# Performance work log

Hardware: AMD Instinct MI355X
Metric: run time of the kernel (lower is better)

The kernel has to match this reference:

```python
import jax, jax.numpy as jnp
import numpy as np

N = 50000
E = 800000
D_IN = 128
H = 128
D_OUT = 64
BN_EPS = 1e-5


def setup_inputs() -> dict:
    key = jax.random.key(0)
    ks = jax.random.split(key, 20)

    def lin(k, fin, fout):
        kw, kb = jax.random.split(k)
        w = jax.random.normal(kw, (fin, fout), jnp.float32) / np.sqrt(fin)
        b = jnp.zeros((fout,), jnp.float32)
        return w, b

    def bn_params(k, d):
        kg, kb = jax.random.split(k)
        g = 1.0 + 0.1 * jax.random.normal(kg, (d,), jnp.float32)
        b = 0.1 * jax.random.normal(kb, (d,), jnp.float32)
        rm = 0.1 * jax.random.normal(jax.random.fold_in(k, 7), (d,), jnp.float32)
        rv = jnp.abs(1.0 + 0.1 * jax.random.normal(jax.random.fold_in(k, 9), (d,), jnp.float32))
        return g, b, rm, rv

    x = jax.random.normal(ks[0], (N, D_IN), jnp.float32)
    edge_index = jax.random.randint(ks[1], (2, E), 0, N, jnp.int64)
    ricci_curvature = jax.random.normal(ks[2], (E,), jnp.float32)

    W1, b1 = lin(ks[3], D_IN, H)
    Wc0, bc0 = lin(ks[4], H, H)          # convs[0]: hidden*1 -> hidden
    Wc1, bc1 = lin(ks[5], 2 * H, H)      # convs[1]: hidden*2 -> hidden
    Wout, bout = lin(ks[6], 3 * H, D_OUT)  # conv2: hidden*(L-1) -> out

    bn1_g, bn1_b, bn1_rm, bn1_rv = bn_params(ks[7], D_IN)
    bnc0_g, bnc0_b, bnc0_rm, bnc0_rv = bn_params(ks[8], H)
    bnc1_g, bnc1_b, bnc1_rm, bnc1_rv = bn_params(ks[9], 2 * H)
    bn2_g, bn2_b, bn2_rm, bn2_rv = bn_params(ks[10], 3 * H)

    return {
        "x": x, "edge_index": edge_index, "percent": 50,
        "ricci_curvature": ricci_curvature,
        "W1": W1, "b1": b1, "Wc0": Wc0, "bc0": bc0,
        "Wc1": Wc1, "bc1": bc1, "Wout": Wout, "bout": bout,
        "bn1_g": bn1_g, "bn1_b": bn1_b, "bn1_rm": bn1_rm, "bn1_rv": bn1_rv,
        "bnc0_g": bnc0_g, "bnc0_b": bnc0_b, "bnc0_rm": bnc0_rm, "bnc0_rv": bnc0_rv,
        "bnc1_g": bnc1_g, "bnc1_b": bnc1_b, "bnc1_rm": bnc1_rm, "bnc1_rv": bnc1_rv,
        "bn2_g": bn2_g, "bn2_b": bn2_b, "bn2_rm": bn2_rm, "bn2_rv": bn2_rv,
    }


def _bn_eval(h, g, b, rm, rv):
    # BatchNorm1d in eval mode: affine normalize with running stats.
    return (h - rm) * (g * jax.lax.rsqrt(rv + BN_EPS)) + b


def reference(x, edge_index, percent, ricci_curvature,
              W1, b1, Wc0, bc0, Wc1, bc1, Wout, bout,
              bn1_g, bn1_b, bn1_rm, bn1_rv,
              bnc0_g, bnc0_b, bnc0_rm, bnc0_rv,
              bnc1_g, bnc1_b, bnc1_rm, bnc1_rv,
              bn2_g, bn2_b, bn2_rm, bn2_rv):
    n = x.shape[0]
    # GCN normalization with self-loops (PyG GCNConv default), shared by all layers
    loops = jnp.arange(n, dtype=edge_index.dtype)
    row = jnp.concatenate([edge_index[0], loops])  # source
    col = jnp.concatenate([edge_index[1], loops])  # target
    deg = jax.ops.segment_sum(jnp.ones_like(col, dtype=x.dtype), col, num_segments=n)
    dinv = jax.lax.rsqrt(deg)  # deg >= 1 thanks to self loops
    norm = (dinv[row] * dinv[col])[:, None]  # [E+N, 1]

    def gcn(h, W, b):
        hw = h @ W                                   # transform first (PyG order)
        msg = hw[row] * norm                          # gather + scale per edge
        return jax.ops.segment_sum(msg, col, num_segments=n) + b

    # eval mode: no sampling / dynamic reweighting, dropout = identity
    h = _bn_eval(x, bn1_g, bn1_b, bn1_rm, bn1_rv)
    h = jax.nn.relu(gcn(h, W1, b1))
    r0 = h

    h = _bn_eval(h, bnc0_g, bnc0_b, bnc0_rm, bnc0_rv)
    h = jax.nn.relu(gcn(h, Wc0, bc0))
    r1 = h
    h = jnp.concatenate([r0, r1], axis=1)  # [N, 2H]

    h = _bn_eval(h, bnc1_g, bnc1_b, bnc1_rm, bnc1_rv)
    h = jax.nn.relu(gcn(h, Wc1, bc1))
    r2 = h
    h = jnp.concatenate([r0, r1, r2], axis=1)  # [N, 3H]

    h = _bn_eval(h, bn2_g, bn2_b, bn2_rm, bn2_rv)
    out = gcn(h, Wout, bout)
    return (out, r0, r1, r2)
```

## Files before the change

### kernel.cpp

```cpp
#include <hip/hip_runtime.h>
#include <hip/hip_bf16.h>
#include <stdint.h>

#define NN 50000
#define NE 800000

typedef unsigned short ushort8 __attribute__((ext_vector_type(8)));
typedef __bf16 bf16x8 __attribute__((ext_vector_type(8)));
typedef float f32x4 __attribute__((ext_vector_type(4)));

__device__ __forceinline__ float bf2f_bits(unsigned short u) {
  unsigned int x = ((unsigned int)u) << 16;
  float f;
  __builtin_memcpy(&f, &x, 4);
  return f;
}
__device__ __forceinline__ unsigned short f2bf_bits(float f) {
  unsigned int x;
  __builtin_memcpy(&x, &f, 4);
  unsigned int lsb = (x >> 16) & 1u;
  x += 0x7fffu + lsb;
  return (unsigned short)(x >> 16);
}
__device__ __forceinline__ float loadf(const void* base, size_t idx, int isbf) {
  if (isbf) return bf2f_bits(((const unsigned short*)base)[idx]);
  return ((const float*)base)[idx];
}

__global__ void k_sniff(const void* x, const void* ei, int* flags) {
  __shared__ int badbf;
  __shared__ int zodd;
  int tid = threadIdx.x;
  if (tid == 0) { badbf = 0; zodd = 0; }
  __syncthreads();
  unsigned short u = ((const unsigned short*)x)[tid];
  float v = bf2f_bits(u);
  float av = fabsf(v);
  int ok = (av == 0.0f) || (av > 1e-8f && av < 1e8f);
  if (!ok) atomicAdd(&badbf, 1);
  int e32 = ((const int*)ei)[tid];
  if ((tid & 1) && e32 == 0) atomicAdd(&zodd, 1);
  __syncthreads();
  if (tid == 0) {
    flags[0] = (badbf <= 12) ? 1 : 0;
    flags[1] = (zodd >= 100) ? 1 : 0;
  }
}

__global__ void k_cvt_edges(const void* ei, int* erow, int* ecol, int* rank,
                            int* cnt, const int* flags) {
  int e = blockIdx.x * 256 + threadIdx.x;
  if (e >= NE) return;
  int r, c;
  if (flags[1]) {
    const long long* p = (const long long*)ei;
    r = (int)p[e];
    c = (int)p[NE + e];
  } else {
    const int* p = (const int*)ei;
    r = p[e];
    c = p[NE + e];
  }
  erow[e] = r;
  ecol[e] = c;
  rank[e] = atomicAdd(&cnt[c], 1);
}

__global__ void k_cvt_xb(const void* x, unsigned short* xb, const int* flags) {
  int i4 = (blockIdx.x * 256 + threadIdx.x) * 4;
  if (i4 >= NN * 128) return;
  int isbf = flags[0];
  if (isbf) {
    *reinterpret_cast<uint2*>(xb + i4) =
        *reinterpret_cast<const uint2*>((const unsigned short*)x + i4);
  } else {
    float4 v = *reinterpret_cast<const float4*>((const float*)x + i4);
    xb[i4 + 0] = f2bf_bits(v.x); xb[i4 + 1] = f2bf_bits(v.y);
    xb[i4 + 2] = f2bf_bits(v.z); xb[i4 + 3] = f2bf_bits(v.w);
  }
}

__global__ void k_zero_int(int* p, int n) {
  int i = blockIdx.x * 256 + threadIdx.x;
  if (i < n) p[i] = 0;
}
__global__ void k_scan1(const int* cnt, int* indptr, int* bsum, float* dinv, int n) {
  __shared__ int sm[256];
  int tid = threadIdx.x;
  int i = blockIdx.x * 256 + tid;
  int v = (i < n) ? cnt[i] : 0;
  if (i < n) dinv[i] = rsqrtf((float)(v + 1));
  sm[tid] = v;
  __syncthreads();
  for (int off = 1; off < 256; off <<= 1) {
    int t = (tid >= off) ? sm[tid - off] : 0;
    __syncthreads();
    sm[tid] += t;
    __syncthreads();
  }
  if (i < n) indptr[i] = sm[tid] - v;
  if (tid == 255) bsum[blockIdx.x] = sm[255];
}
__global__ void k_scan2(int* bsum, int nb) {
  __shared__ int sm[256];
  int tid = threadIdx.x;
  int v = (tid < nb) ? bsum[tid] : 0;
  sm[tid] = v;
  __syncthreads();
  for (int off = 1; off < 256; off <<= 1) {
    int t = (tid >= off) ? sm[tid - off] : 0;
    __syncthreads();
    sm[tid] += t;
    __syncthreads();
  }
  if (tid < nb) bsum[tid] = sm[tid] - v;
  if (tid == 0) bsum[nb] = sm[255];
}
__global__ void k_scan3(int* indptr, const int* bsum, int n, int nb) {
  int i = blockIdx.x * 256 + threadIdx.x;
  if (i < n) indptr[i] += bsum[i >> 8];
  else if (i == n) indptr[n] = bsum[nb];
}
__global__ void k_fill(const int* erow, const int* ecol, const int* rank,
                       const int* indptr, int* srcs) {
  int e = blockIdx.x * 256 + threadIdx.x;
  if (e >= NE) return;
  srcs[indptr[ecol[e]] + rank[e]] = erow[e];
}

__global__ void k_prep_wt_all(
    const void* W1, const void* Wc0, const void* Wc1, const void* Wout,
    const void* g1, const void* g2, const void* g3, const void* g4,
    const void* rv1, const void* rv2, const void* rv3, const void* rv4,
    unsigned short* Wtb, const int* flags) {
  int idx = blockIdx.x * 256 + threadIdx.x;
  if (idx >= 90112) return;
  int isbf = flags[0];
  const void *W, *g, *rv;
  int K, NOUT, base;
  if (idx < 16384)      { W = W1;   g = g1; rv = rv1; K = 128; NOUT = 128; base = 0; }
  else if (idx < 32768) { W = Wc0;  g = g2; rv = rv2; K = 128; NOUT = 128; base = 16384; }
  else if (idx < 65536) { W = Wc1;  g = g3; rv = rv3; K = 256; NOUT = 128; base = 32768; }
  else                  { W = Wout; g = g4; rv = rv4; K = 384; NOUT = 64;  base = 65536; }
  int li = idx - base;
  int j = li / K, k = li % K;
  float s = loadf(g, k, isbf) * rsqrtf(loadf(rv, k, isbf) + 1e-5f);
  Wtb[idx] = f2bf_bits(s * loadf(W, (size_t)k * NOUT + j, isbf));
}
__global__ void k_prep_c_all(
    const void* W1, const void* Wc0, const void* Wc1, const void* Wout,
    const void* g1, const void* g2, const void* g3, const void* g4,
    const void* b1, const void* b2, const void* b3, const void* b4,
    const void* rm1, const void* rm2, const void* rm3, const void* rm4,
    const void* rv1, const void* rv2, const void* rv3, const void* rv4,
    float* cvec, const int* flags) {
  int jj = blockIdx.x;
  int lane = threadIdx.x;
  int isbf = flags[0];
  const void *W, *g, *bb, *rm, *rv;
  int K, NOUT, j;
  if (jj < 128)      { W = W1;   g = g1; bb = b1; rm = rm1; rv = rv1; K = 128; NOUT = 128; j = jj; }
  else if (jj < 256) { W = Wc0;  g = g2; bb = b2; rm = rm2; rv = rv2; K = 128; NOUT = 128; j = jj - 128; }
  else if (jj < 384) { W = Wc1;  g = g3; bb = b3; rm = rm3; rv = rv3; K = 256; NOUT = 128; j = jj - 256; }
  else               { W = Wout; g = g4; bb = b4; rm = rm4; rv = rv4; K = 384; NOUT = 64;  j = jj - 384; }
  float acc = 0.f;
  for (int k = lane; k < K; k += 64) {
    float s = loadf(g, k, isbf) * rsqrtf(loadf(rv, k, isbf) + 1e-5f);
    float t = loadf(bb, k, isbf) - loadf(rm, k, isbf) * s;
    acc += t * loadf(W, (size_t)k * NOUT + j, isbf);
  }
#pragma unroll
  for (int off = 32; off; off >>= 1) acc += __shfl_down(acc, off);
  if (lane == 0) cvec[jj] = acc;
}

template <int NOUT, int K>
__global__ __launch_bounds__(256) void k_gemm_mfma(
    const unsigned short* __restrict__ h0, const unsigned short* __restrict__ h1,
    const unsigned short* __restrict__ h2, const unsigned short* __restrict__ Wtb,
    const float* __restrict__ cvec, const float* __restrict__ dinv,
    unsigned short* __restrict__ hb) {
  constexpr int KS = K / 32;
  constexpr int NT = NOUT / 16;
  int tid = threadIdx.x;
  int wv = tid >> 6, lane = tid & 63;
  int row0 = blockIdx.x * 64 + wv * 16;
  int l15 = lane & 15;
  int kq = lane >> 4;
  int arow = row0 + l15;
  bool inb = arow < NN;

  bf16x8 afrag[KS];
#pragma unroll
  for (int ks = 0; ks < KS; ++ks) {
    int kg = ks * 32 + kq * 8;
    const unsigned short* src = (kg >> 7) == 0 ? h0 : ((kg >> 7) == 1 ? h1 : h2);
    ushort8 u = (ushort8)0;
    if (inb) u = *reinterpret_cast<const ushort8*>(src + (size_t)arow * 128 + (kg & 127));
    afrag[ks] = __builtin_bit_cast(bf16x8, u);
  }

  f32x4 acc[NT];
#pragma unroll
  for (int nt = 0; nt < NT; ++nt) acc[nt] = (f32x4)0.f;

#pragma unroll
  for (int nt = 0; nt < NT; ++nt) {
    const unsigned short* wrow = Wtb + (size_t)(nt * 16 + l15) * K + kq * 8;
#pragma unroll
    for (int ks = 0; ks < KS; ++ks) {
      ushort8 u = *reinterpret_cast<const ushort8*>(wrow + ks * 32);
      acc[nt] = __builtin_amdgcn_mfma_f32_16x16x32_bf16(
          afrag[ks], __builtin_bit_cast(bf16x8, u), acc[nt], 0, 0, 0);
    }
  }

  int orow0 = row0 + kq * 4;
  float dv[4];
  bool ob[4];
#pragma unroll
  for (int r = 0; r < 4; ++r) {
    int orow = orow0 + r;
    ob[r] = orow < NN;
    dv[r] = ob[r] ? dinv[orow] : 0.f;
  }
#pragma unroll
  for (int nt = 0; nt < NT; ++nt) {
    int col = nt * 16 + l15;
    float cv = cvec[col];
#pragma unroll
    for (int r = 0; r < 4; ++r) {
      if (ob[r])
        hb[(size_t)(orow0 + r) * NOUT + col] = f2bf_bits(dv[r] * (acc[nt][r] + cv));
    }
  }
}

template <int DPL, bool RELU>
__global__ __launch_bounds__(256) void k_agg(
    const unsigned short* __restrict__ hb, const int* __restrict__ indptr,
    const int* __restrict__ srcs, const float* __restrict__ dinv,
    const void* __restrict__ bias, void* __restrict__ dout, size_t region_off,
    unsigned short* __restrict__ rb, const int* __restrict__ flags) {
  int gw = blockIdx.x * 8 + (threadIdx.x >> 5);
  int lane = threadIdx.x & 31;
  if (gw >= NN) return;
  int isbf = flags[0];
  int e0 = indptr[gw], e1 = indptr[gw + 1];
  int e = e0;
  float dv = dinv[gw];

  if constexpr (DPL == 2) {
    size_t co = (size_t)lane * 4;
    uint2 sv = *reinterpret_cast<const uint2*>(hb + (size_t)gw * 128 + co);
    float a0 = bf2f_bits((unsigned short)sv.x), a1 = bf2f_bits((unsigned short)(sv.x >> 16));
    float a2 = bf2f_bits((unsigned short)sv.y), a3 = bf2f_bits((unsigned short)(sv.y >> 16));
    float b0 = 0.f, b1 = 0.f, b2 = 0.f, b3 = 0.f;
    float c0 = 0.f, c1 = 0.f, c2 = 0.f, c3 = 0.f;
    float d0 = 0.f, d1 = 0.f, d2 = 0.f, d3 = 0.f;
    for (; e + 3 < e1; e += 4) {
      int sa = srcs[e], sb = srcs[e + 1], sc = srcs[e + 2], sd = srcs[e + 3];
      uint2 va = *reinterpret_cast<const uint2*>(hb + (size_t)sa * 128 + co);
      uint2 vb = *reinterpret_cast<const uint2*>(hb + (size_t)sb * 128 + co);
      uint2 vc = *reinterpret_cast<const uint2*>(hb + (size_t)sc * 128 + co);
      uint2 vd = *reinterpret_cast<const uint2*>(hb + (size_t)sd * 128 + co);
      a0 += bf2f_bits((unsigned short)va.x); a1 += bf2f_bits((unsigned short)(va.x >> 16));
      a2 += bf2f_bits((unsigned short)va.y); a3 += bf2f_bits((unsigned short)(va.y >> 16));
      b0 += bf2f_bits((unsigned short)vb.x); b1 += bf2f_bits((unsigned short)(vb.x >> 16));
      b2 += bf2f_bits((unsigned short)vb.y); b3 += bf2f_bits((unsigned short)(vb.y >> 16));
      c0 += bf2f_bits((unsigned short)vc.x); c1 += bf2f_bits((unsigned short)(vc.x >> 16));
      c2 += bf2f_bits((unsigned short)vc.y); c3 += bf2f_bits((unsigned short)(vc.y >> 16));
      d0 += bf2f_bits((unsigned short)vd.x); d1 += bf2f_bits((unsigned short)(vd.x >> 16));
      d2 += bf2f_bits((unsigned short)vd.y); d3 += bf2f_bits((unsigned short)(vd.y >> 16));
    }
    for (; e < e1; ++e) {
      int sa = srcs[e];
      uint2 va = *reinterpret_cast<const uint2*>(hb + (size_t)sa * 128 + co);
      a0 += bf2f_bits((unsigned short)va.x); a1 += bf2f_bits((unsigned short)(va.x >> 16));
      a2 += bf2f_bits((unsigned short)va.y); a3 += bf2f_bits((unsigned short)(va.y >> 16));
    }
    float o0 = dv * ((a0 + b0) + (c0 + d0)) + loadf(bias, co + 0, isbf);
    float o1 = dv * ((a1 + b1) + (c1 + d1)) + loadf(bias, co + 1, isbf);
    float o2 = dv * ((a2 + b2) + (c2 + d2)) + loadf(bias, co + 2, isbf);
    float o3 = dv * ((a3 + b3) + (c3 + d3)) + loadf(bias, co + 3, isbf);
    if (RELU) {
      o0 = fmaxf(o0, 0.f); o1 = fmaxf(o1, 0.f);
      o2 = fmaxf(o2, 0.f); o3 = fmaxf(o3, 0.f);
    }
    size_t eo = region_off + (size_t)gw * 128 + co;
    uint2 pk;
    pk.x = (unsigned int)f2bf_bits(o0) | ((unsigned int)f2bf_bits(o1) << 16);
    pk.y = (unsigned int)f2bf_bits(o2) | ((unsigned int)f2bf_bits(o3) << 16);
    if (isbf) {
      *reinterpret_cast<uint2*>((unsigned short*)dout + eo) = pk;
    } else {
      float4 fo; fo.x = o0; fo.y = o1; fo.z = o2; fo.w = o3;
      *reinterpret_cast<float4*>((float*)dout + eo) = fo;
    }
    if (rb) *reinterpret_cast<uint2*>(rb + (size_t)gw * 128 + co) = pk;
  } else {
    size_t co = (size_t)lane * 2;
    unsigned int sv = *reinterpret_cast<const unsigned int*>(hb + (size_t)gw * 64 + co);
    float a0 = bf2f_bits((unsigned short)sv), a1 = bf2f_bits((unsigned short)(sv >> 16));
    float b0 = 0.f, b1 = 0.f, c0 = 0.f, c1 = 0.f, d0 = 0.f, d1 = 0.f;
    for (; e + 3 < e1; e += 4) {
      int sa = srcs[e], sb = srcs[e + 1], sc = srcs[e + 2], sd = srcs[e + 3];
      unsigned int va = *reinterpret_cast<const unsigned int*>(hb + (size_t)sa * 64 + co);
      unsigned int vb = *reinterpret_cast<const unsigned int*>(hb + (size_t)sb * 64 + co);
      unsigned int vc = *reinterpret_cast<const unsigned int*>(hb + (size_t)sc * 64 + co);
      unsigned int vd = *reinterpret_cast<const unsigned int*>(hb + (size_t)sd * 64 + co);
      a0 += bf2f_bits((unsigned short)va); a1 += bf2f_bits((unsigned short)(va >> 16));
      b0 += bf2f_bits((unsigned short)vb); b1 += bf2f_bits((unsigned short)(vb >> 16));
      c0 += bf2f_bits((unsigned short)vc); c1 += bf2f_bits((unsigned short)(vc >> 16));
      d0 += bf2f_bits((unsigned short)vd); d1 += bf2f_bits((unsigned short)(vd >> 16));
    }
    for (; e < e1; ++e) {
      int sa = srcs[e];
      unsigned int va = *reinterpret_cast<const unsigned int*>(hb + (size_t)sa * 64 + co);
      a0 += bf2f_bits((unsigned short)va); a1 += bf2f_bits((unsigned short)(va >> 16));
    }
    float o0 = dv * ((a0 + b0) + (c0 + d0)) + loadf(bias, co + 0, isbf);
    float o1 = dv * ((a1 + b1) + (c1 + d1)) + loadf(bias, co + 1, isbf);
    if (RELU) { o0 = fmaxf(o0, 0.f); o1 = fmaxf(o1, 0.f); }
    size_t eo = region_off + (size_t)gw * 64 + co;
    if (isbf) {
      unsigned int pk = (unsigned int)f2bf_bits(o0) | ((unsigned int)f2bf_bits(o1) << 16);
      *reinterpret_cast<unsigned int*>((unsigned short*)dout + eo) = pk;
    } else {
      float2 fo; fo.x = o0; fo.y = o1;
      *reinterpret_cast<float2*>((float*)dout + eo) = fo;
    }
    if (rb) {
      unsigned int pk = (unsigned int)f2bf_bits(o0) | ((unsigned int)f2bf_bits(o1) << 16);
      *reinterpret_cast<unsigned int*>(rb + (size_t)gw * 64 + co) = pk;
    }
  }
}

extern "C" void kernel_launch(void* const* d_in, const int* in_sizes, int n_in,
                              void* d_out, int out_size, void* d_ws, size_t ws_size,
                              hipStream_t stream) {
  const void* x    = d_in[0];
  const void* ei   = d_in[1];
  const void* W1   = d_in[4];
  const void* b1   = d_in[5];
  const void* Wc0  = d_in[6];
  const void* bc0  = d_in[7];
  const void* Wc1  = d_in[8];
  const void* bc1  = d_in[9];
  const void* Wout = d_in[10];
  const void* bout = d_in[11];
  const void *bn1g = d_in[12], *bn1b = d_in[13], *bn1rm = d_in[14], *bn1rv = d_in[15];
  const void *bc0g = d_in[16], *bc0b = d_in[17], *bc0rm = d_in[18], *bc0rv = d_in[19];
  const void *bc1g = d_in[20], *bc1b = d_in[21], *bc1rm = d_in[22], *bc1rv = d_in[23];
  const void *bn2g = d_in[24], *bn2b = d_in[25], *bn2rm = d_in[26], *bn2rv = d_in[27];
  (void)in_sizes; (void)n_in; (void)out_size; (void)ws_size;

  char* w = (char*)d_ws;
  auto carve = [&](size_t bytes) {
    char* p = w;
    w += (bytes + 255) & ~(size_t)255;
    return p;
  };
  int*   flags  = (int*)  carve(256);
  float* dinv   = (float*)carve(sizeof(float) * NN);
  int*   cnt    = (int*)  carve(sizeof(int) * NN);
  int*   indptr = (int*)  carve(sizeof(int) * (NN + 1));
  int*   bsum   = (int*)  carve(sizeof(int) * 256);
  int*   erow   = (int*)  carve(sizeof(int) * NE);
  int*   ecol   = (int*)  carve(sizeof(int) * NE);
  int*   rank   = (int*)  carve(sizeof(int) * NE);
  int*   srcs   = (int*)  carve(sizeof(int) * NE);
  unsigned short* Wtb = (unsigned short*)carve(sizeof(short) * 90112);
  float* cvec   = (float*)carve(sizeof(float) * 448);
  unsigned short* xb  = (unsigned short*)carve(sizeof(short) * (size_t)NN * 128);
  unsigned short* hb  = (unsigned short*)carve(sizeof(short) * (size_t)NN * 128);
  unsigned short* rb0 = (unsigned short*)carve(sizeof(short) * (size_t)NN * 128);
  unsigned short* rb1 = (unsigned short*)carve(sizeof(short) * (size_t)NN * 128);
  unsigned short* rb2 = (unsigned short*)carve(sizeof(short) * (size_t)NN * 128);

  const int gN = (NN + 255) / 256;
  const int gE = (NE + 255) / 256;
  const int nb = (NN + 255) / 256;
  const int gG = (NN + 63) / 64;
  const int gA = (NN + 7) / 8;

  k_sniff<<<1, 256, 0, stream>>>(x, ei, flags);
  k_zero_int<<<gN, 256, 0, stream>>>(cnt, NN);
  k_cvt_edges<<<gE, 256, 0, stream>>>(ei, erow, ecol, rank, cnt, flags);
  k_cvt_xb<<<(NN * 128 / 4 + 255) / 256, 256, 0, stream>>>(x, xb, flags);
  k_scan1<<<nb, 256, 0, stream>>>(cnt, indptr, bsum, dinv, NN);
  k_scan2<<<1, 256, 0, stream>>>(bsum, nb);
  k_scan3<<<(NN + 1 + 255) / 256, 256, 0, stream>>>(indptr, bsum, NN, nb);
  k_fill<<<gE, 256, 0, stream>>>(erow, ecol, rank, indptr, srcs);
  k_prep_wt_all<<<(90112 + 255) / 256, 256, 0, stream>>>(
      W1, Wc0, Wc1, Wout, bn1g, bc0g, bc1g, bn2g, bn1rv, bc0rv, bc1rv, bn2rv, Wtb, flags);
  k_prep_c_all<<<448, 64, 0, stream>>>(
      W1, Wc0, Wc1, Wout, bn1g, bc0g, bc1g, bn2g, bn1b, bc0b, bc1b, bn2b,
      bn1rm, bc0rm, bc1rm, bn2rm, bn1rv, bc0rv, bc1rv, bn2rv, cvec, flags);

  const size_t offO  = 0;
  const size_t offR0 = (size_t)NN * 64;
  const size_t offR1 = offR0 + (size_t)NN * 128;
  const size_t offR2 = offR1 + (size_t)NN * 128;

  k_gemm_mfma<128, 128><<<gG, 256, 0, stream>>>(xb, nullptr, nullptr, Wtb + 0, cvec + 0, dinv, hb);
  k_agg<2, true><<<gA, 256, 0, stream>>>(hb, indptr, srcs, dinv, b1, d_out, offR0, rb0, flags);

  k_gemm_mfma<128, 128><<<gG, 256, 0, stream>>>(rb0, nullptr, nullptr, Wtb + 16384, cvec + 128, dinv, hb);
  k_agg<2, true><<<gA, 256, 0, stream>>>(hb, indptr, srcs, dinv, bc0, d_out, offR1, rb1, flags);

  k_gemm_mfma<128, 256><<<gG, 256, 0, stream>>>(rb0, rb1, nullptr, Wtb + 32768, cvec + 256, dinv, hb);
  k_agg<2, true><<<gA, 256, 0, stream>>>(hb, indptr, srcs, dinv, bc1, d_out, offR2, rb2, flags);

  k_gemm_mfma<64, 384><<<gG, 256, 0, stream>>>(rb0, rb1, rb2, Wtb + 65536, cvec + 384, dinv, hb);
  k_agg<1, false><<<gA, 256, 0, stream>>>(hb, indptr, srcs, dinv, bout, d_out, offO, nullptr, flags);
}
```

Before: 340.4 us.

## Use wave64 per node for 128-wide aggregation and skip redundant bf16 residual copies

The 128-wide aggregation now assigns a full 64-lane wave per node, with each lane handling 2 features and 8 edges unrolled per iteration, where before 32 lanes handled 4 features each. When the output is bf16, the aggregation no longer writes a separate bf16 residual buffer; the following GEMMs read the residuals directly from the output tensor. The count-zeroing kernel is folded into the sniff kernel to save a launch. In exchange, each edge now costs smaller 4-byte gathers per lane and there are more waves per node count.

Measured after the change: 334.4 us. Within noise of the previous version (-1.8%).

```diff
diff --git a/kernel.cpp b/kernel.cpp
--- a/kernel.cpp
+++ b/kernel.cpp
@@ -22,12 +22,17 @@
   x += 0x7fffu + lsb;
   return (unsigned short)(x >> 16);
 }
+__device__ __forceinline__ float lo16(unsigned int v) { return bf2f_bits((unsigned short)v); }
+__device__ __forceinline__ float hi16(unsigned int v) { return bf2f_bits((unsigned short)(v >> 16)); }
 __device__ __forceinline__ float loadf(const void* base, size_t idx, int isbf) {
   if (isbf) return bf2f_bits(((const unsigned short*)base)[idx]);
   return ((const float*)base)[idx];
 }
 
-__global__ void k_sniff(const void* x, const void* ei, int* flags) {
+__global__ void k_sniff(const void* x, const void* ei, int* flags, int* cnt) {
+  int i = blockIdx.x * 256 + threadIdx.x;
+  if (i < NN) cnt[i] = 0;
+  if (blockIdx.x != 0) return;
   __shared__ int badbf;
   __shared__ int zodd;
   int tid = threadIdx.x;
@@ -80,10 +85,6 @@
   }
 }
 
-__global__ void k_zero_int(int* p, int n) {
-  int i = blockIdx.x * 256 + threadIdx.x;
-  if (i < n) p[i] = 0;
-}
 __global__ void k_scan1(const int* cnt, int* indptr, int* bsum, float* dinv, int n) {
   __shared__ int sm[256];
   int tid = threadIdx.x;
@@ -176,12 +177,19 @@
 
 template <int NOUT, int K>
 __global__ __launch_bounds__(256) void k_gemm_mfma(
-    const unsigned short* __restrict__ h0, const unsigned short* __restrict__ h1,
-    const unsigned short* __restrict__ h2, const unsigned short* __restrict__ Wtb,
+    const unsigned short* __restrict__ h0b, const unsigned short* __restrict__ h1b,
+    const unsigned short* __restrict__ h2b,
+    const unsigned short* __restrict__ h0d, const unsigned short* __restrict__ h1d,
+    const unsigned short* __restrict__ h2d,
+    const unsigned short* __restrict__ Wtb,
     const float* __restrict__ cvec, const float* __restrict__ dinv,
-    unsigned short* __restrict__ hb) {
+    unsigned short* __restrict__ hb, const int* __restrict__ flags) {
   constexpr int KS = K / 32;
   constexpr int NT = NOUT / 16;
+  int isbf = flags[0];
+  const unsigned short* h0 = (isbf && h0d) ? h0d : h0b;
+  const unsigned short* h1 = (isbf && h1d) ? h1d : h1b;
+  const unsigned short* h2 = (isbf && h2d) ? h2d : h2b;
   int tid = threadIdx.x;
   int wv = tid >> 6, lane = tid & 63;
   int row0 = blockIdx.x * 64 + wv * 16;
@@ -236,104 +244,98 @@
   }
 }
 
-template <int DPL, bool RELU>
-__global__ __launch_bounds__(256) void k_agg(
+template <bool RELU>
+__global__ __launch_bounds__(256) void k_agg128(
     const unsigned short* __restrict__ hb, const int* __restrict__ indptr,
     const int* __restrict__ srcs, const float* __restrict__ dinv,
     const void* __restrict__ bias, void* __restrict__ dout, size_t region_off,
     unsigned short* __restrict__ rb, const int* __restrict__ flags) {
+  int gw = __builtin_amdgcn_readfirstlane(blockIdx.x * 4 + (threadIdx.x >> 6));
+  int lane = threadIdx.x & 63;
+  if (gw >= NN) return;
+  int isbf = flags[0];
+  int e0 = indptr[gw], e1 = indptr[gw + 1];
+  size_t co = (size_t)lane * 2;
+  unsigned int sv = *reinterpret_cast<const unsigned int*>(hb + (size_t)gw * 128 + co);
+  float a0 = lo16(sv), a1 = hi16(sv);
+  float b0 = 0.f, b1 = 0.f, c0 = 0.f, c1 = 0.f, d0 = 0.f, d1 = 0.f;
+  int e = e0;
+  for (; e + 7 < e1; e += 8) {
+    int s0 = srcs[e], s1 = srcs[e + 1], s2 = srcs[e + 2], s3 = srcs[e + 3];
+    int s4 = srcs[e + 4], s5 = srcs[e + 5], s6 = srcs[e + 6], s7 = srcs[e + 7];
+    unsigned int v0 = *reinterpret_cast<const unsigned int*>(hb + (size_t)s0 * 128 + co);
+    unsigned int v1 = *reinterpret_cast<const unsigned int*>(hb + (size_t)s1 * 128 + co);
+    unsigned int v2 = *reinterpret_cast<const unsigned int*>(hb + (size_t)s2 * 128 + co);
+    unsigned int v3 = *reinterpret_cast<const unsigned int*>(hb + (size_t)s3 * 128 + co);
+    unsigned int v4 = *reinterpret_cast<const unsigned int*>(hb + (size_t)s4 * 128 + co);
+    unsigned int v5 = *reinterpret_cast<const unsigned int*>(hb + (size_t)s5 * 128 + co);
+    unsigned int v6 = *reinterpret_cast<const unsigned int*>(hb + (size_t)s6 * 128 + co);
+    unsigned int v7 = *reinterpret_cast<const unsigned int*>(hb + (size_t)s7 * 128 + co);
+    a0 += lo16(v0); a1 += hi16(v0); b0 += lo16(v1); b1 += hi16(v1);
+    c0 += lo16(v2); c1 += hi16(v2); d0 += lo16(v3); d1 += hi16(v3);
+    a0 += lo16(v4); a1 += hi16(v4); b0 += lo16(v5); b1 += hi16(v5);
+    c0 += lo16(v6); c1 += hi16(v6); d0 += lo16(v7); d1 += hi16(v7);
+  }
+  for (; e < e1; ++e) {
+    int s0 = srcs[e];
+    unsigned int v0 = *reinterpret_cast<const unsigned int*>(hb + (size_t)s0 * 128 + co);
+    a0 += lo16(v0); a1 += hi16(v0);
+  }
+  float dv = dinv[gw];
+  float o0 = dv * ((a0 + b0) + (c0 + d0)) + loadf(bias, co + 0, isbf);
+  float o1 = dv * ((a1 + b1) + (c1 + d1)) + loadf(bias, co + 1, isbf);
+  if (RELU) { o0 = fmaxf(o0, 0.f); o1 = fmaxf(o1, 0.f); }
+  size_t eo = region_off + (size_t)gw * 128 + co;
+  if (isbf) {
+    unsigned int pk = (unsigned int)f2bf_bits(o0) | ((unsigned int)f2bf_bits(o1) << 16);
+    *reinterpret_cast<unsigned int*>((unsigned short*)dout + eo) = pk;
+  } else {
+    float2 fo; fo.x = o0; fo.y = o1;
+    *reinterpret_cast<float2*>((float*)dout + eo) = fo;
+    unsigned int pk = (unsigned int)f2bf_bits(o0) | ((unsigned int)f2bf_bits(o1) << 16);
+    *reinterpret_cast<unsigned int*>(rb + (size_t)gw * 128 + co) = pk;
+  }
+}
+
+__global__ __launch_bounds__(256) void k_agg64out(
+    const unsigned short* __restrict__ hb, const int* __restrict__ indptr,
+    const int* __restrict__ srcs, const float* __restrict__ dinv,
+    const void* __restrict__ bias, void* __restrict__ dout,
+    const int* __restrict__ flags) {
   int gw = blockIdx.x * 8 + (threadIdx.x >> 5);
   int lane = threadIdx.x & 31;
   if (gw >= NN) return;
   int isbf = flags[0];
   int e0 = indptr[gw], e1 = indptr[gw + 1];
   int e = e0;
+  size_t co = (size_t)lane * 2;
+  unsigned int sv = *reinterpret_cast<const unsigned int*>(hb + (size_t)gw * 64 + co);
+  float a0 = lo16(sv), a1 = hi16(sv);
+  float b0 = 0.f, b1 = 0.f, c0 = 0.f, c1 = 0.f, d0 = 0.f, d1 = 0.f;
+  for (; e + 3 < e1; e += 4) {
+    int sa = srcs[e], sb = srcs[e + 1], sc = srcs[e + 2], sd = srcs[e + 3];
+    unsigned int va = *reinterpret_cast<const unsigned int*>(hb + (size_t)sa * 64 + co);
+    unsigned int vb = *reinterpret_cast<const unsigned int*>(hb + (size_t)sb * 64 + co);
+    unsigned int vc = *reinterpret_cast<const unsigned int*>(hb + (size_t)sc * 64 + co);
+    unsigned int vd = *reinterpret_cast<const unsigned int*>(hb + (size_t)sd * 64 + co);
+    a0 += lo16(va); a1 += hi16(va); b0 += lo16(vb); b1 += hi16(vb);
+    c0 += lo16(vc); c1 += hi16(vc); d0 += lo16(vd); d1 += hi16(vd);
+  }
+  for (; e < e1; ++e) {
+    int sa = srcs[e];
+    unsigned int va = *reinterpret_cast<const unsigned int*>(hb + (size_t)sa * 64 + co);
+    a0 += lo16(va); a1 += hi16(va);
+  }
   float dv = dinv[gw];
-
-  if constexpr (DPL == 2) {
-    size_t co = (size_t)lane * 4;
-    uint2 sv = *reinterpret_cast<const uint2*>(hb + (size_t)gw * 128 + co);
-    float a0 = bf2f_bits((unsigned short)sv.x), a1 = bf2f_bits((unsigned short)(sv.x >> 16));
-    float a2 = bf2f_bits((unsigned short)sv.y), a3 = bf2f_bits((unsigned short)(sv.y >> 16));
-    float b0 = 0.f, b1 = 0.f, b2 = 0.f, b3 = 0.f;
-    float c0 = 0.f, c1 = 0.f, c2 = 0.f, c3 = 0.f;
-    float d0 = 0.f, d1 = 0.f, d2 = 0.f, d3 = 0.f;
-    for (; e + 3 < e1; e += 4) {
-      int sa = srcs[e], sb = srcs[e + 1], sc = srcs[e + 2], sd = srcs[e + 3];
-      uint2 va = *reinterpret_cast<const uint2*>(hb + (size_t)sa * 128 + co);
-      uint2 vb = *reinterpret_cast<const uint2*>(hb + (size_t)sb * 128 + co);
-      uint2 vc = *reinterpret_cast<const uint2*>(hb + (size_t)sc * 128 + co);
-      uint2 vd = *reinterpret_cast<const uint2*>(hb + (size_t)sd * 128 + co);
-      a0 += bf2f_bits((unsigned short)va.x); a1 += bf2f_bits((unsigned short)(va.x >> 16));
-      a2 += bf2f_bits((unsigned short)va.y); a3 += bf2f_bits((unsigned short)(va.y >> 16));
-      b0 += bf2f_bits((unsigned short)vb.x); b1 += bf2f_bits((unsigned short)(vb.x >> 16));
-      b2 += bf2f_bits((unsigned short)vb.y); b3 += bf2f_bits((unsigned short)(vb.y >> 16));
-      c0 += bf2f_bits((unsigned short)vc.x); c1 += bf2f_bits((unsigned short)(vc.x >> 16));
-      c2 += bf2f_bits((unsigned short)vc.y); c3 += bf2f_bits((unsigned short)(vc.y >> 16));
-      d0 += bf2f_bits((unsigned short)vd.x); d1 += bf2f_bits((unsigned short)(vd.x >> 16));
-      d2 += bf2f_bits((unsigned short)vd.y); d3 += bf2f_bits((unsigned short)(vd.y >> 16));
-    }
-    for (; e < e1; ++e) {
-      int sa = srcs[e];
-      uint2 va = *reinterpret_cast<const uint2*>(hb + (size_t)sa * 128 + co);
-      a0 += bf2f_bits((unsigned short)va.x); a1 += bf2f_bits((unsigned short)(va.x >> 16));
-      a2 += bf2f_bits((unsigned short)va.y); a3 += bf2f_bits((unsigned short)(va.y >> 16));
-    }
-    float o0 = dv * ((a0 + b0) + (c0 + d0)) + loadf(bias, co + 0, isbf);
-    float o1 = dv * ((a1 + b1) + (c1 + d1)) + loadf(bias, co + 1, isbf);
-    float o2 = dv * ((a2 + b2) + (c2 + d2)) + loadf(bias, co + 2, isbf);
-    float o3 = dv * ((a3 + b3) + (c3 + d3)) + loadf(bias, co + 3, isbf);
-    if (RELU) {
-      o0 = fmaxf(o0, 0.f); o1 = fmaxf(o1, 0.f);
-      o2 = fmaxf(o2, 0.f); o3 = fmaxf(o3, 0.f);
-    }
-    size_t eo = region_off + (size_t)gw * 128 + co;
-    uint2 pk;
-    pk.x = (unsigned int)f2bf_bits(o0) | ((unsigned int)f2bf_bits(o1) << 16);
-    pk.y = (unsigned int)f2bf_bits(o2) | ((unsigned int)f2bf_bits(o3) << 16);
-    if (isbf) {
-      *reinterpret_cast<uint2*>((unsigned short*)dout + eo) = pk;
-    } else {
-      float4 fo; fo.x = o0; fo.y = o1; fo.z = o2; fo.w = o3;
-      *reinterpret_cast<float4*>((float*)dout + eo) = fo;
-    }
-    if (rb) *reinterpret_cast<uint2*>(rb + (size_t)gw * 128 + co) = pk;
+  float o0 = dv * ((a0 + b0) + (c0 + d0)) + loadf(bias, co + 0, isbf);
+  float o1 = dv * ((a1 + b1) + (c1 + d1)) + loadf(bias, co + 1, isbf);
+  size_t eo = (size_t)gw * 64 + co;
+  if (isbf) {
+    unsigned int pk = (unsigned int)f2bf_bits(o0) | ((unsigned int)f2bf_bits(o1) << 16);
+    *reinterpret_cast<unsigned int*>((unsigned short*)dout + eo) = pk;
   } else {
-    size_t co = (size_t)lane * 2;
-    unsigned int sv = *reinterpret_cast<const unsigned int*>(hb + (size_t)gw * 64 + co);
-    float a0 = bf2f_bits((unsigned short)sv), a1 = bf2f_bits((unsigned short)(sv >> 16));
-    float b0 = 0.f, b1 = 0.f, c0 = 0.f, c1 = 0.f, d0 = 0.f, d1 = 0.f;
-    for (; e + 3 < e1; e += 4) {
-      int sa = srcs[e], sb = srcs[e + 1], sc = srcs[e + 2], sd = srcs[e + 3];
-      unsigned int va = *reinterpret_cast<const unsigned int*>(hb + (size_t)sa * 64 + co);
-      unsigned int vb = *reinterpret_cast<const unsigned int*>(hb + (size_t)sb * 64 + co);
-      unsigned int vc = *reinterpret_cast<const unsigned int*>(hb + (size_t)sc * 64 + co);
-      unsigned int vd = *reinterpret_cast<const unsigned int*>(hb + (size_t)sd * 64 + co);
-      a0 += bf2f_bits((unsigned short)va); a1 += bf2f_bits((unsigned short)(va >> 16));
-      b0 += bf2f_bits((unsigned short)vb); b1 += bf2f_bits((unsigned short)(vb >> 16));
-      c0 += bf2f_bits((unsigned short)vc); c1 += bf2f_bits((unsigned short)(vc >> 16));
-      d0 += bf2f_bits((unsigned short)vd); d1 += bf2f_bits((unsigned short)(vd >> 16));
-    }
-    for (; e < e1; ++e) {
-      int sa = srcs[e];
-      unsigned int va = *reinterpret_cast<const unsigned int*>(hb + (size_t)sa * 64 + co);
-      a0 += bf2f_bits((unsigned short)va); a1 += bf2f_bits((unsigned short)(va >> 16));
-    }
-    float o0 = dv * ((a0 + b0) + (c0 + d0)) + loadf(bias, co + 0, isbf);
-    float o1 = dv * ((a1 + b1) + (c1 + d1)) + loadf(bias, co + 1, isbf);
-    if (RELU) { o0 = fmaxf(o0, 0.f); o1 = fmaxf(o1, 0.f); }
-    size_t eo = region_off + (size_t)gw * 64 + co;
-    if (isbf) {
-      unsigned int pk = (unsigned int)f2bf_bits(o0) | ((unsigned int)f2bf_bits(o1) << 16);
-      *reinterpret_cast<unsigned int*>((unsigned short*)dout + eo) = pk;
-    } else {
-      float2 fo; fo.x = o0; fo.y = o1;
-      *reinterpret_cast<float2*>((float*)dout + eo) = fo;
-    }
-    if (rb) {
-      unsigned int pk = (unsigned int)f2bf_bits(o0) | ((unsigned int)f2bf_bits(o1) << 16);
-      *reinterpret_cast<unsigned int*>(rb + (size_t)gw * 64 + co) = pk;
-    }
+    float2 fo; fo.x = o0; fo.y = o1;
+    *reinterpret_cast<float2*>((float*)dout + eo) = fo;
   }
 }
 
@@ -383,10 +385,10 @@
   const int gE = (NE + 255) / 256;
   const int nb = (NN + 255) / 256;
   const int gG = (NN + 63) / 64;
-  const int gA = (NN + 7) / 8;
-
-  k_sniff<<<1, 256, 0, stream>>>(x, ei, flags);
-  k_zero_int<<<gN, 256, 0, stream>>>(cnt, NN);
+  const int gA2 = (NN + 3) / 4;
+  const int gA1 = (NN + 7) / 8;
+
+  k_sniff<<<gN, 256, 0, stream>>>(x, ei, flags, cnt);
   k_cvt_edges<<<gE, 256, 0, stream>>>(ei, erow, ecol, rank, cnt, flags);
   k_cvt_xb<<<(NN * 128 / 4 + 255) / 256, 256, 0, stream>>>(x, xb, flags);
   k_scan1<<<nb, 256, 0, stream>>>(cnt, indptr, bsum, dinv, NN);
@@ -403,16 +405,21 @@
   const size_t offR0 = (size_t)NN * 64;
   const size_t offR1 = offR0 + (size_t)NN * 128;
   const size_t offR2 = offR1 + (size_t)NN * 128;
-
-  k_gemm_mfma<128, 128><<<gG, 256, 0, stream>>>(xb, nullptr, nullptr, Wtb + 0, cvec + 0, dinv, hb);
-  k_agg<2, true><<<gA, 256, 0, stream>>>(hb, indptr, srcs, dinv, b1, d_out, offR0, rb0, flags);
-
-  k_gemm_mfma<128, 128><<<gG, 256, 0, stream>>>(rb0, nullptr, nullptr, Wtb + 16384, cvec + 128, dinv, hb);
-  k_agg<2, true><<<gA, 256, 0, stream>>>(hb, indptr, srcs, dinv, bc0, d_out, offR1, rb1, flags);
-
-  k_gemm_mfma<128, 256><<<gG, 256, 0, stream>>>(rb0, rb1, nullptr, Wtb + 32768, cvec + 256, dinv, hb);
-  k_agg<2, true><<<gA, 256, 0, stream>>>(hb, indptr, srcs, dinv, bc1, d_out, offR2, rb2, flags);
-
-  k_gemm_mfma<64, 384><<<gG, 256, 0, stream>>>(rb0, rb1, rb2, Wtb + 65536, cvec + 384, dinv, hb);
-  k_agg<1, false><<<gA, 256, 0, stream>>>(hb, indptr, srcs, dinv, bout, d_out, offO, nullptr, flags);
-}
+  unsigned short* d0 = (unsigned short*)d_out;
+
+  k_gemm_mfma<128, 128><<<gG, 256, 0, stream>>>(
+      xb, nullptr, nullptr, nullptr, nullptr, nullptr, Wtb + 0, cvec + 0, dinv, hb, flags);
+  k_agg128<true><<<gA2, 256, 0, stream>>>(hb, indptr, srcs, dinv, b1, d_out, offR0, rb0, flags);
+
+  k_gemm_mfma<128, 128><<<gG, 256, 0, stream>>>(
+      rb0, nullptr, nullptr, d0 + offR0, nullptr, nullptr, Wtb + 16384, cvec + 128, dinv, hb, flags);
+  k_agg128<true><<<gA2, 256, 0, stream>>>(hb, indptr, srcs, dinv, bc0, d_out, offR1, rb1, flags);
+
+  k_gemm_mfma<128, 256><<<gG, 256, 0, stream>>>(
+      rb0, rb1, nullptr, d0 + offR0, d0 + offR1, nullptr, Wtb + 32768, cvec + 256, dinv, hb, flags);
+  k_agg128<true><<<gA2, 256, 0, stream>>>(hb, indptr, srcs, dinv, bc1, d_out, offR2, rb2, flags);
+
+  k_gemm_mfma<64, 384><<<gG, 256, 0, stream>>>(
+      rb0, rb1, rb2, d0 + offR0, d0 + offR1, d0 + offR2, Wtb + 65536, cvec + 384, dinv, hb, flags);
+  k_agg64out<<<gA1, 256, 0, stream>>>(hb, indptr, srcs, dinv, bout, d_out, flags);
+}
```
